# Kernel tuning notes

Hardware: AMD Instinct MI355X
Metric: run time of the kernel (lower is better)

## Reference

```python
import jax, jax.numpy as jnp
import numpy as np
import math

B, S, DIM, H = 4, 1024, 4096, 32
HD = DIM // H  # head_dim = 128
MAX_B, MAX_S = 4, 1024
START_POS = 0
ROPE_THETA = 10000.0


def setup_inputs() -> dict:
    key = jax.random.key(0)
    ks = jax.random.split(key, 6)
    x = jax.random.normal(ks[0], (B, S, DIM), dtype=jnp.float32)
    # real RoPE frequencies: freqs_cis[t, j] = exp(i * t * theta^{-2j/hd})
    inv_freq = 1.0 / (ROPE_THETA ** (jnp.arange(0, HD, 2, dtype=jnp.float32) / HD))  # [HD/2]
    t = jnp.arange(START_POS, START_POS + S, dtype=jnp.float32)
    ang = jnp.outer(t, inv_freq)  # [S, HD/2]
    freqs_cos = jnp.cos(ang)
    freqs_sin = jnp.sin(ang)
    # additive causal mask as in llama: -inf above diagonal offset start_pos+1
    mask = jnp.triu(jnp.full((1, 1, S, S), float('-inf'), dtype=jnp.float32), k=START_POS + 1)
    scale = 0.02
    wq = jax.random.normal(ks[1], (DIM, DIM), dtype=jnp.float32) * scale
    wk = jax.random.normal(ks[2], (DIM, DIM), dtype=jnp.float32) * scale
    wv = jax.random.normal(ks[3], (DIM, DIM), dtype=jnp.float32) * scale
    wo = jax.random.normal(ks[4], (DIM, DIM), dtype=jnp.float32) * scale
    cache_k = jnp.zeros((MAX_B, MAX_S, H, HD), dtype=jnp.float32)
    cache_v = jnp.zeros((MAX_B, MAX_S, H, HD), dtype=jnp.float32)
    return {"x": x, "start_pos": START_POS, "freqs_cos": freqs_cos, "freqs_sin": freqs_sin,
            "mask": mask, "wq": wq, "wk": wk, "wv": wv, "wo": wo,
            "cache_k": cache_k, "cache_v": cache_v}


def _apply_rotary(t, cos, sin):
    # t: [B, S, H, HD]; interpret last dim as HD/2 complex pairs (real, imag)
    b, s, h, d = t.shape
    tr = t.reshape(b, s, h, d // 2, 2)
    a, bb = tr[..., 0], tr[..., 1]
    c = cos[None, :, None, :]  # [1, S, 1, HD/2]
    si = sin[None, :, None, :]
    out_r = a * c - bb * si
    out_i = a * si + bb * c
    return jnp.stack([out_r, out_i], axis=-1).reshape(b, s, h, d)


def reference(x, start_pos, freqs_cos, freqs_sin, mask, wq, wk, wv, wo, cache_k, cache_v):
    bsz, seqlen, dim = x.shape
    hd = HD
    # torch Linear: y = x @ W.T, W is [out, in]
    xq = (x @ wq.T).reshape(bsz, seqlen, H, hd)
    xk = (x @ wk.T).reshape(bsz, seqlen, H, hd)
    xv = (x @ wv.T).reshape(bsz, seqlen, H, hd)
    xq = _apply_rotary(xq, freqs_cos, freqs_sin)
    xk = _apply_rotary(xk, freqs_cos, freqs_sin)
    # KV-cache write
    cache_k = jax.lax.dynamic_update_slice(cache_k, xk, (0, start_pos, 0, 0))
    cache_v = jax.lax.dynamic_update_slice(cache_v, xv, (0, start_pos, 0, 0))
    keys = cache_k[:bsz, :start_pos + seqlen]    # [B, K, H, HD]
    values = cache_v[:bsz, :start_pos + seqlen]  # [B, K, H, HD]
    # naive attention: full score matrix
    scores = jnp.einsum('bqhd,bkhd->bhqk', xq, keys) / math.sqrt(hd)
    scores = scores + mask
    probs = jax.nn.softmax(scores.astype(jnp.float32), axis=-1).astype(xq.dtype)
    out = jnp.einsum('bhqk,bkhd->bqhd', probs, values)
    out = out.reshape(bsz, seqlen, -1)
    return out @ wo.T
```

## Files before the change

### kernel.cpp

```cpp
#include <hip/hip_runtime.h>
#include <hip/hip_bf16.h>
#include <cstdint>

typedef __hip_bfloat16 bf16;
typedef __attribute__((ext_vector_type(8))) short frag8;
typedef __attribute__((ext_vector_type(4))) float f32x4;

#define DEV __device__ __forceinline__

DEV void gl_lds16(const void* g, void* l) {
  __builtin_amdgcn_global_load_lds(
      (const __attribute__((address_space(1))) void*)g,
      (__attribute__((address_space(3))) void*)l, 16, 0, 0);
}

DEV void storeC(float* C, size_t idx, float v) { C[idx] = v; }
DEV void storeC(bf16* C, size_t idx, float v) { C[idx] = __float2bfloat16(v); }

__global__ __launch_bounds__(256) void conv_kernel(const float* __restrict__ in,
                                                   bf16* __restrict__ out, int n8) {
  int i = blockIdx.x * 256 + threadIdx.x;
  if (i >= n8) return;
  const float4* in4 = reinterpret_cast<const float4*>(in);
  float4 a = in4[2 * i], b = in4[2 * i + 1];
  union { frag8 v; bf16 h[8]; } u;
  u.h[0] = __float2bfloat16(a.x); u.h[1] = __float2bfloat16(a.y);
  u.h[2] = __float2bfloat16(a.z); u.h[3] = __float2bfloat16(a.w);
  u.h[4] = __float2bfloat16(b.x); u.h[5] = __float2bfloat16(b.y);
  u.h[6] = __float2bfloat16(b.z); u.h[7] = __float2bfloat16(b.w);
  *reinterpret_cast<frag8*>(out + (size_t)i * 8) = u.v;
}

#define MF(a, b, c) __builtin_amdgcn_mfma_f32_16x16x32_bf16(a, b, c, 0, 0, 0)

#define STAGE(isB, h, tt, bp) do {                                             \
    char* _d = lds + ((isB) * 65536) + ((((bp) * 2) + (h)) << 14);             \
    gl_lds16(((isB) ? gB : gA)[h][0] + (size_t)(tt) * 64, _d + ldsOff0);       \
    gl_lds16(((isB) ? gB : gA)[h][1] + (size_t)(tt) * 64, _d + ldsOff1);       \
  } while (0)

#define RDA(mi, ckk) (*(const frag8*)(ab + aRowB + (mi) * 2048 + (ckk)))
#define RDB(ni, ckk) (*(const frag8*)(bb + bRowB + (ni) * 2048 + (ckk)))

#define PHASE(p, SSTAGE, SWAIT) do {                                           \
    if ((p) == 0) {                                                            \
      b00 = RDB(0, ck0); b01 = RDB(0, ck1); b10 = RDB(1, ck0); b11 = RDB(1, ck1); \
      b20 = RDB(2, ck0); b21 = RDB(2, ck1); b30 = RDB(3, ck0); b31 = RDB(3, ck1); \
    }                                                                          \
    frag8 a00 = RDA(2 * (p), ck0), a01 = RDA(2 * (p), ck1);                    \
    frag8 a10 = RDA(2 * (p) + 1, ck0), a11 = RDA(2 * (p) + 1, ck1);            \
    SSTAGE;                                                                    \
    SWAIT;                                                                     \
    __builtin_amdgcn_s_barrier();                                              \
    __builtin_amdgcn_s_setprio(1);                                             \
    acc[2*(p)][0]   = MF(a00, b00, acc[2*(p)][0]);                             \
    acc[2*(p)][1]   = MF(a00, b10, acc[2*(p)][1]);                             \
    acc[2*(p)][2]   = MF(a00, b20, acc[2*(p)][2]);                             \
    acc[2*(p)][3]   = MF(a00, b30, acc[2*(p)][3]);                             \
    acc[2*(p)+1][0] = MF(a10, b00, acc[2*(p)+1][0]);                           \
    acc[2*(p)+1][1] = MF(a10, b10, acc[2*(p)+1][1]);                           \
    acc[2*(p)+1][2] = MF(a10, b20, acc[2*(p)+1][2]);                           \
    acc[2*(p)+1][3] = MF(a10, b30, acc[2*(p)+1][3]);                           \
    acc[2*(p)][0]   = MF(a01, b01, acc[2*(p)][0]);                             \
    acc[2*(p)][1]   = MF(a01, b11, acc[2*(p)][1]);                             \
    acc[2*(p)][2]   = MF(a01, b21, acc[2*(p)][2]);                             \
    acc[2*(p)][3]   = MF(a01, b31, acc[2*(p)][3]);                             \
    acc[2*(p)+1][0] = MF(a11, b01, acc[2*(p)+1][0]);                           \
    acc[2*(p)+1][1] = MF(a11, b11, acc[2*(p)+1][1]);                           \
    acc[2*(p)+1][2] = MF(a11, b21, acc[2*(p)+1][2]);                           \
    acc[2*(p)+1][3] = MF(a11, b31, acc[2*(p)+1][3]);                           \
    __builtin_amdgcn_s_setprio(0);                                             \
    __builtin_amdgcn_s_barrier();                                              \
  } while (0)

#define VM4 asm volatile("s_waitcnt vmcnt(4)" ::: "memory")
#define VM0 asm volatile("s_waitcnt vmcnt(0)" ::: "memory")
#define NOW ((void)0)

#define TILE(t, SA, SB, SWAIT) do {                                            \
    const int _bp2 = ((t) & 1) * 2;                                            \
    char* ab = lds + ((_bp2 + wm) << 14);                                      \
    char* bb = lds + 65536 + ((_bp2 + bhalf) << 14);                           \
    PHASE(0, { if (SA) STAGE(0, 0, (t) + 1, ((t) + 1) & 1); }, NOW);           \
    PHASE(1, { if (SA) STAGE(0, 1, (t) + 1, ((t) + 1) & 1); }, NOW);           \
    PHASE(2, { if (SB) STAGE(1, 0, (t) + 2, (t) & 1); }, NOW);                 \
    PHASE(3, { if (SB) STAGE(1, 1, (t) + 2, (t) & 1); }, SWAIT);               \
  } while (0)

template <typename OutT>
__global__ __launch_bounds__(512, 2) void gemm8(const bf16* __restrict__ A,
                                                const bf16* __restrict__ Bt,
                                                OutT* __restrict__ C) {
  __shared__ __align__(16) char lds[131072];
  const int K = 4096, N = 4096;
  const int t = threadIdx.x;
  const int lane = t & 63, w = t >> 6;
  const int wm = w >> 2, wn = w & 3;
  const int lr = lane & 15, lg = lane >> 4;
  const int bhalf = wn >> 1;

  const int bid = blockIdx.x;
  const int wg = (bid & 7) * 32 + (bid >> 3);
  const int m0 = (wg >> 4) * 256, n0 = (wg & 15) * 256;

  const bf16* gA[2][2];
  const bf16* gB[2][2];
  int ldsOff0, ldsOff1;
  {
    int c0 = (w * 2 + 0) * 64 + lane;
    int c1 = (w * 2 + 1) * 64 + lane;
    int r0 = c0 >> 3, r1 = c1 >> 3;
    int e0 = ((c0 & 7) ^ (r0 & 7)) * 8;
    int e1 = ((c1 & 7) ^ (r1 & 7)) * 8;
    ldsOff0 = c0 * 16; ldsOff1 = c1 * 16;
    gA[0][0] = A + (size_t)(m0 + r0) * K + e0;
    gA[0][1] = A + (size_t)(m0 + r1) * K + e1;
    gA[1][0] = A + (size_t)(m0 + 128 + r0) * K + e0;
    gA[1][1] = A + (size_t)(m0 + 128 + r1) * K + e1;
    gB[0][0] = Bt + (size_t)(n0 + r0) * K + e0;
    gB[0][1] = Bt + (size_t)(n0 + r1) * K + e1;
    gB[1][0] = Bt + (size_t)(n0 + 128 + r0) * K + e0;
    gB[1][1] = Bt + (size_t)(n0 + 128 + r1) * K + e1;
  }

  const int swz = (lr & 7) << 4;
  const int ck0 = (lg * 16) ^ swz;
  const int ck1 = (64 + lg * 16) ^ swz;
  const int aRowB = lr * 128;
  const int bRowB = ((wn & 1) * 64 + lr) * 128;

  f32x4 acc[8][4];
#pragma unroll
  for (int mi = 0; mi < 8; ++mi)
#pragma unroll
    for (int ni = 0; ni < 4; ++ni) acc[mi][ni] = (f32x4){0.f, 0.f, 0.f, 0.f};

  frag8 b00, b01, b10, b11, b20, b21, b30, b31;

  STAGE(1, 0, 0, 0); STAGE(1, 1, 0, 0);
  STAGE(0, 0, 0, 0); STAGE(0, 1, 0, 0);
  STAGE(1, 0, 1, 1); STAGE(1, 1, 1, 1);
  VM4;
  __builtin_amdgcn_s_barrier();

  for (int tt = 0; tt < 62; tt += 2) {
    TILE(tt, 1, 1, VM4);
    TILE(tt + 1, 1, 1, VM4);
  }
  TILE(62, 1, 0, VM0);
  TILE(63, 0, 0, NOW);

#pragma unroll
  for (int mi = 0; mi < 8; ++mi)
#pragma unroll
    for (int ni = 0; ni < 4; ++ni) {
      f32x4 v = acc[mi][ni];
      int col = n0 + wn * 64 + ni * 16 + lr;
#pragma unroll
      for (int i = 0; i < 4; ++i) {
        int row = m0 + wm * 128 + mi * 16 + lg * 4 + i;
        storeC(C, (size_t)row * N + col, v[i]);
      }
    }
}

__global__ __launch_bounds__(256) void rope_kernel(bf16* __restrict__ q, bf16* __restrict__ k,
                                                   const float* __restrict__ fc,
                                                   const float* __restrict__ fs) {
  int idx = blockIdx.x * 256 + threadIdx.x;
  int i = idx & 63;
  int s = (idx >> 11) & 1023;
  float c = fc[s * 64 + i], sn = fs[s * 64 + i];
  uint32_t* qp = reinterpret_cast<uint32_t*>(q) + idx;
  uint32_t* kp = reinterpret_cast<uint32_t*>(k) + idx;
  union { uint32_t u; bf16 h[2]; } a, r;
  a.u = *qp;
  {
    float x = __bfloat162float(a.h[0]), y = __bfloat162float(a.h[1]);
    r.h[0] = __float2bfloat16(x * c - y * sn);
    r.h[1] = __float2bfloat16(x * sn + y * c);
    *qp = r.u;
  }
  a.u = *kp;
  {
    float x = __bfloat162float(a.h[0]), y = __bfloat162float(a.h[1]);
    r.h[0] = __float2bfloat16(x * c - y * sn);
    r.h[1] = __float2bfloat16(x * sn + y * c);
    *kp = r.u;
  }
}

__global__ __launch_bounds__(256) void transpose_v_kernel(const bf16* __restrict__ v,
                                                          bf16* __restrict__ vt) {
  __shared__ unsigned short tile[32][40];
  const int st = blockIdx.x * 32;
  const int dt = blockIdx.y * 32;
  const int bh = blockIdx.z;
  const int b = bh >> 5, h = bh & 31;
  const int t = threadIdx.x;
  const int r = t >> 3, c4 = (t & 7) * 4;
  const unsigned short* src = reinterpret_cast<const unsigned short*>(v) +
      ((size_t)(b * 1024 + st + r)) * 4096 + h * 128 + dt + c4;
  uint2 d = *reinterpret_cast<const uint2*>(src);
  tile[r][c4 + 0] = (unsigned short)(d.x & 0xffff);
  tile[r][c4 + 1] = (unsigned short)(d.x >> 16);
  tile[r][c4 + 2] = (unsigned short)(d.y & 0xffff);
  tile[r][c4 + 3] = (unsigned short)(d.y >> 16);
  __syncthreads();
  uint2 o;
  o.x = (uint32_t)tile[c4 + 0][r] | ((uint32_t)tile[c4 + 1][r] << 16);
  o.y = (uint32_t)tile[c4 + 2][r] | ((uint32_t)tile[c4 + 3][r] << 16);
  unsigned short* dst = reinterpret_cast<unsigned short*>(vt) +
      ((size_t)bh * 128 + dt + r) * 1024 + st + c4;
  *reinterpret_cast<uint2*>(dst) = o;
}

__global__ __launch_bounds__(512, 4) void attn_kernel(const bf16* __restrict__ q,
                                                      const bf16* __restrict__ k,
                                                      const bf16* __restrict__ vt,
                                                      bf16* __restrict__ out) {
  __shared__ __align__(16) char als[81920];
  const int qt = blockIdx.x, h = blockIdx.y, b = blockIdx.z;
  const int t = threadIdx.x;
  const int lane = t & 63, w = t >> 6;
  const int lr = lane & 15, lg = lane >> 4;
  const int NT = 2 * qt + 2;

  frag8 aq[4];
  {
    const bf16* qp = q + ((size_t)(b * 1024 + qt * 128 + w * 16 + lr)) * 4096 + h * 128 + lg * 8;
#pragma unroll
    for (int ks = 0; ks < 4; ++ks) aq[ks] = *reinterpret_cast<const frag8*>(qp + ks * 32);
  }

  const bf16* kbase = k + (size_t)b * 1024 * 4096 + h * 128;
  const bf16* vbase = vt + ((size_t)(b * 32 + h)) * 128 * 1024;

  const int L0 = t * 16, L1 = (t + 512) * 16;
  const int kr0 = L0 >> 8, kr1 = L1 >> 8;
  const size_t kOff0 = (size_t)kr0 * 4096 + (((L0 & 255) ^ ((kr0 & 7) << 4)) >> 1);
  const size_t kOff1 = (size_t)kr1 * 4096 + (((L1 & 255) ^ ((kr1 & 7) << 4)) >> 1);
  const int vr0 = L0 >> 7, vr1 = L1 >> 7;
  const size_t vOff0 = (size_t)vr0 * 1024 + (((L0 & 127) ^ ((vr0 & 7) << 4)) >> 1);
  const size_t vOff1 = (size_t)vr1 * 1024 + (((L1 & 127) ^ ((vr1 & 7) << 4)) >> 1);

#define STAGE_K(tt, bp) do { char* _d = als + (bp) * 16384;                    \
    gl_lds16(kbase + (size_t)(tt) * 262144 + kOff0, _d + L0);                  \
    gl_lds16(kbase + (size_t)(tt) * 262144 + kOff1, _d + L1); } while (0)
#define STAGE_V(tt, bp) do { char* _d = als + 32768 + (bp) * 16384;            \
    gl_lds16(vbase + (size_t)(tt) * 64 + vOff0, _d + L0);                      \
    gl_lds16(vbase + (size_t)(tt) * 64 + vOff1, _d + L1); } while (0)

  f32x4 oacc[8] = {};
  float mrow[4] = {-1e30f, -1e30f, -1e30f, -1e30f};
  float lrow[4] = {0.f, 0.f, 0.f, 0.f};
  char* Pw = als + 65536 + w * 2048;
  const float scale = 0.08838834764831845f;
  const int qmaxw = qt * 128 + w * 16 + 15;

  STAGE_K(0, 0); STAGE_V(0, 0);
  STAGE_K(1, 1); STAGE_V(1, 1);

  for (int kt = 0; kt < NT; ++kt) {
    const int cur = kt & 1;
    const bool act = (kt * 64 <= qmaxw);
    const bool domask = (kt >= 2 * qt);
    char* Kc = als + cur * 16384;
    char* Vc = als + 32768 + cur * 16384;

    if (kt + 1 < NT) { VM4; } else { VM0; }
    __builtin_amdgcn_s_barrier();

    f32x4 sacc[4] = {};
    if (act) {
      __builtin_amdgcn_s_setprio(1);
#pragma unroll
      for (int ks = 0; ks < 4; ++ks) {
#pragma unroll
        for (int ni = 0; ni < 4; ++ni) {
          int n = ni * 16 + lr;
          frag8 bk = *reinterpret_cast<const frag8*>(
              Kc + n * 256 + ((ks * 64 + lg * 16) ^ ((n & 7) << 4)));
          sacc[ni] = MF(aq[ks], bk, sacc[ni]);
        }
      }
      __builtin_amdgcn_s_setprio(0);
    }
    __builtin_amdgcn_s_barrier();
    if (kt + 2 < NT) STAGE_K(kt + 2, cur);

    if (act) {
#pragma unroll
      for (int ni = 0; ni < 4; ++ni)
#pragma unroll
        for (int i = 0; i < 4; ++i) {
          float x = sacc[ni][i] * scale;
          if (domask) {
            int qr = qt * 128 + w * 16 + lg * 4 + i;
            int kc = kt * 64 + ni * 16 + lr;
            if (kc > qr) x = -1e30f;
          }
          sacc[ni][i] = x;
        }

      float fs_[4];
#pragma unroll
      for (int i = 0; i < 4; ++i) {
        float pm = fmaxf(fmaxf(sacc[0][i], sacc[1][i]), fmaxf(sacc[2][i], sacc[3][i]));
#pragma unroll
        for (int m = 1; m <= 8; m <<= 1) pm = fmaxf(pm, __shfl_xor(pm, m));
        float mn = fmaxf(mrow[i], pm);
        float f = __expf(mrow[i] - mn);
        float rs = 0.f;
#pragma unroll
        for (int ni = 0; ni < 4; ++ni) {
          float p = __expf(sacc[ni][i] - mn);
          sacc[ni][i] = p;
          rs += p;
        }
#pragma unroll
        for (int m = 1; m <= 8; m <<= 1) rs += __shfl_xor(rs, m);
        lrow[i] = lrow[i] * f + rs;
        mrow[i] = mn;
        fs_[i] = f;
      }
#pragma unroll
      for (int nj = 0; nj < 8; ++nj)
#pragma unroll
        for (int i = 0; i < 4; ++i) oacc[nj][i] *= fs_[i];

#pragma unroll
      for (int ni = 0; ni < 4; ++ni)
#pragma unroll
        for (int i = 0; i < 4; ++i) {
          int prow = lg * 4 + i;
          int pb = prow * 128 + (((ni * 16 + lr) * 2) ^ ((prow & 7) << 4));
          *reinterpret_cast<bf16*>(Pw + pb) = __float2bfloat16(sacc[ni][i]);
        }

      __builtin_amdgcn_s_setprio(1);
#pragma unroll
      for (int ks2 = 0; ks2 < 2; ++ks2) {
        frag8 ap = *reinterpret_cast<const frag8*>(
            Pw + lr * 128 + ((ks2 * 64 + lg * 16) ^ ((lr & 7) << 4)));
#pragma unroll
        for (int nj = 0; nj < 8; ++nj) {
          int d = nj * 16 + lr;
          frag8 bv = *reinterpret_cast<const frag8*>(
              Vc + d * 128 + ((ks2 * 64 + lg * 16) ^ ((d & 7) << 4)));
          oacc[nj] = MF(ap, bv, oacc[nj]);
        }
      }
      __builtin_amdgcn_s_setprio(0);
    }
    __builtin_amdgcn_s_barrier();
    if (kt + 2 < NT) STAGE_V(kt + 2, cur);
  }

#pragma unroll
  for (int nj = 0; nj < 8; ++nj)
#pragma unroll
    for (int i = 0; i < 4; ++i) {
      int srow = qt * 128 + w * 16 + lg * 4 + i;
      out[((size_t)(b * 1024 + srow)) * 4096 + h * 128 + nj * 16 + lr] =
          __float2bfloat16(oacc[nj][i] / lrow[i]);
    }
#undef STAGE_K
#undef STAGE_V
}

extern "C" void kernel_launch(void* const* d_in, const int* in_sizes, int n_in,
                              void* d_out, int out_size, void* d_ws, size_t ws_size,
                              hipStream_t stream) {
  const float* x  = (const float*)d_in[0];
  const float* fc = (const float*)d_in[2];
  const float* fs = (const float*)d_in[3];
  const float* wq = (const float*)d_in[5];
  const float* wk = (const float*)d_in[6];
  const float* wv = (const float*)d_in[7];
  const float* wo = (const float*)d_in[8];
  float* out = (float*)d_out;

  const size_t SZ = (size_t)4096 * 4096 * 2;
  char* w = (char*)d_ws;
  bf16* xb = (bf16*)(w);
  bf16* wb = (bf16*)(w + SZ);
  bf16* qb = (bf16*)(w + 2 * SZ);
  bf16* kb = (bf16*)(w + 3 * SZ);
  bf16* vb = (bf16*)(w + 4 * SZ);
  bf16* vtb = xb;
  bf16* ao  = vb;

  const int n8 = 4096 * 4096 / 8;
  dim3 cgrd(n8 / 256), blk(256);
  dim3 ggrd(256);
  dim3 gblk(512);

  conv_kernel<<<cgrd, blk, 0, stream>>>(x, xb, n8);
  conv_kernel<<<cgrd, blk, 0, stream>>>(wq, wb, n8);
  gemm8<bf16><<<ggrd, gblk, 0, stream>>>(xb, wb, qb);
  conv_kernel<<<cgrd, blk, 0, stream>>>(wk, wb, n8);
  gemm8<bf16><<<ggrd, gblk, 0, stream>>>(xb, wb, kb);
  conv_kernel<<<cgrd, blk, 0, stream>>>(wv, wb, n8);
  gemm8<bf16><<<ggrd, gblk, 0, stream>>>(xb, wb, vb);
  rope_kernel<<<dim3(32768), blk, 0, stream>>>(qb, kb, fc, fs);
  transpose_v_kernel<<<dim3(32, 4, 128), blk, 0, stream>>>(vb, vtb);
  attn_kernel<<<dim3(8, 32, 4), gblk, 0, stream>>>(qb, kb, vtb, ao);
  conv_kernel<<<cgrd, blk, 0, stream>>>(wo, wb, n8);
  gemm8<float><<<ggrd, gblk, 0, stream>>>(ao, wb, out);
}
```

Measured before the change: 712.3 us.

## Compute transposed S tile so each lane owns one query row for softmax

Swaps the MFMA operand order for QK^T so the score fragment is transposed, giving each lane one query row with 16 key values. The row max and sum then need two cross-lane shuffles instead of four per row across four rows, and P can be written to LDS as packed 32-bit pairs. The rescale factors and final row sums are broadcast back to the output layout with shuffles. This cuts softmax shuffle and exp bookkeeping overhead at the cost of extra broadcast shuffles.

```diff
diff --git a/kernel.cpp b/kernel.cpp
--- a/kernel.cpp
+++ b/kernel.cpp
@@ -252,11 +252,11 @@
     gl_lds16(vbase + (size_t)(tt) * 64 + vOff1, _d + L1); } while (0)
 
   f32x4 oacc[8] = {};
-  float mrow[4] = {-1e30f, -1e30f, -1e30f, -1e30f};
-  float lrow[4] = {0.f, 0.f, 0.f, 0.f};
+  float mrow = -1e30f, lrow = 0.f;
   char* Pw = als + 65536 + w * 2048;
   const float scale = 0.08838834764831845f;
   const int qmaxw = qt * 128 + w * 16 + 15;
+  const int qr_g = qt * 128 + w * 16 + lr;
 
   STAGE_K(0, 0); STAGE_V(0, 0);
   STAGE_K(1, 1); STAGE_V(1, 1);
@@ -281,7 +281,7 @@
           int n = ni * 16 + lr;
           frag8 bk = *reinterpret_cast<const frag8*>(
               Kc + n * 256 + ((ks * 64 + lg * 16) ^ ((n & 7) << 4)));
-          sacc[ni] = MF(aq[ks], bk, sacc[ni]);
+          sacc[ni] = MF(bk, aq[ks], sacc[ni]);
         }
       }
       __builtin_amdgcn_s_setprio(0);
@@ -296,47 +296,55 @@
         for (int i = 0; i < 4; ++i) {
           float x = sacc[ni][i] * scale;
           if (domask) {
-            int qr = qt * 128 + w * 16 + lg * 4 + i;
-            int kc = kt * 64 + ni * 16 + lr;
-            if (kc > qr) x = -1e30f;
+            int kc = kt * 64 + ni * 16 + lg * 4 + i;
+            if (kc > qr_g) x = -1e30f;
           }
           sacc[ni][i] = x;
         }
 
-      float fs_[4];
-#pragma unroll
-      for (int i = 0; i < 4; ++i) {
-        float pm = fmaxf(fmaxf(sacc[0][i], sacc[1][i]), fmaxf(sacc[2][i], sacc[3][i]));
-#pragma unroll
-        for (int m = 1; m <= 8; m <<= 1) pm = fmaxf(pm, __shfl_xor(pm, m));
-        float mn = fmaxf(mrow[i], pm);
-        float f = __expf(mrow[i] - mn);
-        float rs = 0.f;
-#pragma unroll
-        for (int ni = 0; ni < 4; ++ni) {
+      float pm = sacc[0][0];
+#pragma unroll
+      for (int ni = 0; ni < 4; ++ni)
+#pragma unroll
+        for (int i = 0; i < 4; ++i) pm = fmaxf(pm, sacc[ni][i]);
+      pm = fmaxf(pm, __shfl_xor(pm, 16));
+      pm = fmaxf(pm, __shfl_xor(pm, 32));
+      float mn = fmaxf(mrow, pm);
+      float f = __expf(mrow - mn);
+      float rs = 0.f;
+#pragma unroll
+      for (int ni = 0; ni < 4; ++ni)
+#pragma unroll
+        for (int i = 0; i < 4; ++i) {
           float p = __expf(sacc[ni][i] - mn);
           sacc[ni][i] = p;
           rs += p;
         }
-#pragma unroll
-        for (int m = 1; m <= 8; m <<= 1) rs += __shfl_xor(rs, m);
-        lrow[i] = lrow[i] * f + rs;
-        mrow[i] = mn;
-        fs_[i] = f;
+      rs += __shfl_xor(rs, 16);
+      rs += __shfl_xor(rs, 32);
+      lrow = lrow * f + rs;
+      mrow = mn;
+
+#pragma unroll
+      for (int ni = 0; ni < 4; ++ni)
+#pragma unroll
+        for (int j = 0; j < 2; ++j) {
+          union { uint32_t u; bf16 hh[2]; } pk;
+          pk.hh[0] = __float2bfloat16(sacc[ni][2 * j]);
+          pk.hh[1] = __float2bfloat16(sacc[ni][2 * j + 1]);
+          int kc2 = (ni * 16 + lg * 4 + 2 * j) * 2;
+          *reinterpret_cast<uint32_t*>(Pw + lr * 128 + (kc2 ^ ((lr & 7) << 4))) = pk.u;
+        }
+
+      float fi0 = __shfl(f, lg * 4 + 0);
+      float fi1 = __shfl(f, lg * 4 + 1);
+      float fi2 = __shfl(f, lg * 4 + 2);
+      float fi3 = __shfl(f, lg * 4 + 3);
+#pragma unroll
+      for (int nj = 0; nj < 8; ++nj) {
+        oacc[nj][0] *= fi0; oacc[nj][1] *= fi1;
+        oacc[nj][2] *= fi2; oacc[nj][3] *= fi3;
       }
-#pragma unroll
-      for (int nj = 0; nj < 8; ++nj)
-#pragma unroll
-        for (int i = 0; i < 4; ++i) oacc[nj][i] *= fs_[i];
-
-#pragma unroll
-      for (int ni = 0; ni < 4; ++ni)
-#pragma unroll
-        for (int i = 0; i < 4; ++i) {
-          int prow = lg * 4 + i;
-          int pb = prow * 128 + (((ni * 16 + lr) * 2) ^ ((prow & 7) << 4));
-          *reinterpret_cast<bf16*>(Pw + pb) = __float2bfloat16(sacc[ni][i]);
-        }
 
       __builtin_amdgcn_s_setprio(1);
 #pragma unroll
@@ -357,14 +365,19 @@
     if (kt + 2 < NT) STAGE_V(kt + 2, cur);
   }
 
-#pragma unroll
-  for (int nj = 0; nj < 8; ++nj)
-#pragma unroll
-    for (int i = 0; i < 4; ++i) {
-      int srow = qt * 128 + w * 16 + lg * 4 + i;
-      out[((size_t)(b * 1024 + srow)) * 4096 + h * 128 + nj * 16 + lr] =
-          __float2bfloat16(oacc[nj][i] / lrow[i]);
-    }
+  float lv0 = __shfl(lrow, lg * 4 + 0);
+  float lv1 = __shfl(lrow, lg * 4 + 1);
+  float lv2 = __shfl(lrow, lg * 4 + 2);
+  float lv3 = __shfl(lrow, lg * 4 + 3);
+#pragma unroll
+  for (int nj = 0; nj < 8; ++nj) {
+    int srow0 = qt * 128 + w * 16 + lg * 4;
+    size_t base = ((size_t)(b * 1024 + srow0)) * 4096 + h * 128 + nj * 16 + lr;
+    out[base]          = __float2bfloat16(oacc[nj][0] / lv0);
+    out[base + 4096]   = __float2bfloat16(oacc[nj][1] / lv1);
+    out[base + 8192]   = __float2bfloat16(oacc[nj][2] / lv2);
+    out[base + 12288]  = __float2bfloat16(oacc[nj][3] / lv3);
+  }
 #undef STAGE_K
 #undef STAGE_V
 }
```

New measurement: 686.1 us. -3.7%, faster.
